# Kernel optimization log

Measured on AMD Instinct MI355X. Metric: run time of the kernel, lower is better.

The kernel has to match this reference:

```python
import jax, jax.numpy as jnp
import numpy as np

B, D, H, W = 16, 256, 32, 32
M = 2048


def setup_inputs() -> dict:
    key = jax.random.key(0)
    kz, ke = jax.random.split(key)
    z = jax.random.normal(kz, (B, D, H, W), dtype=jnp.float32)
    e = jax.random.normal(ke, (M, D), dtype=jnp.float32)
    return {"z": z, "e": e}


def reference(z, e):
    # flatten (B, D, H, W) -> (N, D), matching permute(0,2,3,1).reshape(-1, D)
    zf = jnp.transpose(z, (0, 2, 3, 1)).reshape(-1, z.shape[1])  # (N, D)
    # squared L2 distance via GEMM expansion: ||z||^2 + ||e||^2 - 2 z.e^T
    z_sq = jnp.sum(zf * zf, axis=1, keepdims=True)        # (N, 1)
    e_sq = jnp.sum(e * e, axis=1)                          # (M,)
    cross = jnp.einsum('nd,md->nm', zf, e)                 # (N, M)
    distance = jnp.maximum(z_sq + e_sq[None, :] - 2.0 * cross, 0.0)  # (N, M)
    # loss: mean over codes of min over flattened z vectors (min along dim 0)
    loss = jnp.mean(jnp.min(distance, axis=0))
    return distance, loss
```

## Files before the change

kernel.cpp:

```cpp
#include <hip/hip_runtime.h>

typedef __attribute__((ext_vector_type(8))) short bf16x8;
typedef __attribute__((ext_vector_type(4))) float f32x4;

#define NTOT 16384
#define MCODES 2048
#define DDIM 256

__device__ __forceinline__ unsigned short f2bf(float f) {
  union { float f; unsigned u; } v; v.f = f;
  unsigned r = v.u + 0x7FFFu + ((v.u >> 16) & 1u);
  return (unsigned short)(r >> 16);
}

#define GLOAD16(gptr, lptr) \
  __builtin_amdgcn_global_load_lds((const __attribute__((address_space(1))) void*)(gptr), \
                                   (__attribute__((address_space(3))) void*)(lptr), 16, 0, 0)

__global__ void prep_e_k(const float* __restrict__ e, unsigned short* __restrict__ ebf,
                         float* __restrict__ esq, unsigned* __restrict__ colmin,
                         float* __restrict__ zsq) {
  if (blockIdx.x < 64) zsq[blockIdx.x * 256 + threadIdx.x] = 0.0f;
  int row = blockIdx.x * 4 + (threadIdx.x >> 6);
  int lane = threadIdx.x & 63;
  const float4 v = *(const float4*)(e + (size_t)row * DDIM + lane * 4);
  ushort4 o;
  o.x = f2bf(v.x); o.y = f2bf(v.y); o.z = f2bf(v.z); o.w = f2bf(v.w);
  *(ushort4*)(ebf + (size_t)row * DDIM + lane * 4) = o;
  float s = v.x * v.x + v.y * v.y + v.z * v.z + v.w * v.w;
  #pragma unroll
  for (int off = 32; off; off >>= 1) s += __shfl_xor(s, off, 64);
  if (lane == 0) {
    esq[row] = s;
    colmin[row] = 0x7F800000u;
  }
}

__global__ void trans_zsq_k(const float* __restrict__ z, unsigned short* __restrict__ zf,
                            float* __restrict__ zsq) {
  __shared__ float t[64][65];
  const int b = blockIdx.z, d0 = blockIdx.x * 64, hw0 = blockIdx.y * 64;
  const int tid = threadIdx.x;
  {
    const int dl = tid >> 4, hwl = (tid & 15) * 4;
    const float* src = z + (size_t)b * 262144 + (size_t)(d0 + dl) * 1024 + hw0 + hwl;
    #pragma unroll
    for (int it = 0; it < 4; ++it) {
      float4 v = *(const float4*)(src + (size_t)it * 16 * 1024);
      *(float4*)&t[it * 16 + dl][hwl] = v;
    }
  }
  __syncthreads();
  const int hwl = tid >> 3;
  const int dl = (tid & 7) * 8;
  #pragma unroll
  for (int p = 0; p < 2; ++p) {
    const int hw = p * 32 + hwl;
    float vv[8];
    float s = 0.0f;
    #pragma unroll
    for (int u = 0; u < 8; ++u) { vv[u] = t[dl + u][hw]; s += vv[u] * vv[u]; }
    bf16x8 pk;
    #pragma unroll
    for (int u = 0; u < 8; ++u) pk[u] = (short)f2bf(vv[u]);
    const size_t n = (size_t)b * 1024 + hw0 + hw;
    *(bf16x8*)(zf + n * DDIM + d0 + dl) = pk;
    s += __shfl_xor(s, 1, 64);
    s += __shfl_xor(s, 2, 64);
    s += __shfl_xor(s, 4, 64);
    if ((tid & 7) == 0) atomicAdd(zsq + n, s);
  }
}

__global__ __launch_bounds__(256, 2) void gemm_k(
    const unsigned short* __restrict__ A,
    const unsigned short* __restrict__ B,
    const float* __restrict__ zsq, const float* __restrict__ esq,
    unsigned* __restrict__ colmin, float* __restrict__ out) {
  __shared__ unsigned short lds[2][2 * 128 * 64];
  const int tid = threadIdx.x;
  const int wave = tid >> 6, lane = tid & 63;
  const int wm = wave >> 1, wn = wave & 1;
  const int row0 = blockIdx.y * 128, col0 = blockIdx.x * 128;

  const int sr = tid >> 3;
  const int scs = ((tid & 7) * 8) ^ ((sr & 7) * 8);
  size_t aOff[4], bOff[4];
  #pragma unroll
  for (int c = 0; c < 4; ++c) {
    aOff[c] = (size_t)(row0 + c * 32 + sr) * DDIM + scs;
    bOff[c] = (size_t)(col0 + c * 32 + sr) * DDIM + scs;
  }

  const int rA = wm * 64 + (lane & 15);
  const int rB = wn * 64 + (lane & 15);
  const int slot = (lane >> 4) * 16;
  const int swz = (lane & 7) << 4;

  f32x4 acc[4][4] = {};

  #define STAGE(buf, k0)                                                    \
    {                                                                       \
      unsigned short* la = &lds[buf][0];                                    \
      unsigned short* lb = &lds[buf][8192];                                 \
      _Pragma("unroll")                                                     \
      for (int c = 0; c < 4; ++c) {                                         \
        GLOAD16(A + aOff[c] + (k0), la + c * 2048 + wave * 512);            \
        GLOAD16(B + bOff[c] + (k0), lb + c * 2048 + wave * 512);            \
      }                                                                     \
    }

  STAGE(0, 0);
  __syncthreads();
  #pragma unroll
  for (int t = 0; t < 4; ++t) {
    const int cur = t & 1;
    if (t < 3) STAGE(cur ^ 1, (t + 1) * 64);
    const char* pA = (const char*)&lds[cur][0];
    const char* pB = (const char*)&lds[cur][8192];
    bf16x8 av[2][4], bv[2][4];
    #pragma unroll
    for (int kk = 0; kk < 2; ++kk) {
      #pragma unroll
      for (int i = 0; i < 4; ++i)
        av[kk][i] = *(const bf16x8*)(pA + (rA + i * 16) * 128 + ((kk * 64 + slot) ^ swz));
      #pragma unroll
      for (int j = 0; j < 4; ++j)
        bv[kk][j] = *(const bf16x8*)(pB + (rB + j * 16) * 128 + ((kk * 64 + slot) ^ swz));
    }
    #pragma unroll
    for (int kk = 0; kk < 2; ++kk)
      #pragma unroll
      for (int i = 0; i < 4; ++i)
        #pragma unroll
        for (int j = 0; j < 4; ++j)
          acc[i][j] = __builtin_amdgcn_mfma_f32_16x16x32_bf16(av[kk][i], bv[kk][j], acc[i][j], 0, 0, 0);
    if (t < 3) __syncthreads();
  }
  #undef STAGE

  const int r0 = lane >> 4, c = lane & 15;
  float cmin[4] = {3.4e38f, 3.4e38f, 3.4e38f, 3.4e38f};
  #pragma unroll
  for (int j = 0; j < 4; ++j) {
    const int col = col0 + wn * 64 + j * 16 + c;
    const float es = esq[col];
    #pragma unroll
    for (int i = 0; i < 4; ++i) {
      const int row = row0 + wm * 64 + i * 16 + r0 * 4;
      const float4 zs = *(const float4*)(zsq + row);
      const float d0 = fmaxf(zs.x + es - 2.0f * acc[i][j][0], 0.0f);
      const float d1 = fmaxf(zs.y + es - 2.0f * acc[i][j][1], 0.0f);
      const float d2 = fmaxf(zs.z + es - 2.0f * acc[i][j][2], 0.0f);
      const float d3 = fmaxf(zs.w + es - 2.0f * acc[i][j][3], 0.0f);
      __builtin_nontemporal_store(d0, &out[(size_t)(row + 0) * MCODES + col]);
      __builtin_nontemporal_store(d1, &out[(size_t)(row + 1) * MCODES + col]);
      __builtin_nontemporal_store(d2, &out[(size_t)(row + 2) * MCODES + col]);
      __builtin_nontemporal_store(d3, &out[(size_t)(row + 3) * MCODES + col]);
      cmin[j] = fminf(cmin[j], fminf(fminf(d0, d1), fminf(d2, d3)));
    }
  }
  #pragma unroll
  for (int j = 0; j < 4; ++j) {
    float m = cmin[j];
    m = fminf(m, __shfl_xor(m, 16, 64));
    m = fminf(m, __shfl_xor(m, 32, 64));
    if (lane < 16) {
      const int col = col0 + wn * 64 + j * 16 + lane;
      atomicMin(colmin + col, __float_as_uint(m));
    }
  }
}

__global__ void loss_k(const unsigned* __restrict__ colmin, float* __restrict__ loss) {
  __shared__ float sdata[4];
  int t = threadIdx.x;
  float s = 0.0f;
  for (int i = t; i < MCODES; i += 256) s += __uint_as_float(colmin[i]);
  #pragma unroll
  for (int off = 32; off; off >>= 1) s += __shfl_down(s, off, 64);
  if ((t & 63) == 0) sdata[t >> 6] = s;
  __syncthreads();
  if (t == 0) loss[0] = (sdata[0] + sdata[1] + sdata[2] + sdata[3]) * (1.0f / (float)MCODES);
}

extern "C" void kernel_launch(void* const* d_in, const int* in_sizes, int n_in,
                              void* d_out, int out_size, void* d_ws, size_t ws_size,
                              hipStream_t stream) {
  const float* z = (const float*)d_in[0];
  const float* e = (const float*)d_in[1];
  float* out = (float*)d_out;

  float* ws = (float*)d_ws;
  float* zsq = ws;
  float* esq = ws + NTOT;
  unsigned* colmin = (unsigned*)(ws + NTOT + MCODES);
  unsigned short* ebf = (unsigned short*)(ws + NTOT + 2 * MCODES);
  unsigned short* zf = ebf + (size_t)MCODES * DDIM;

  prep_e_k<<<MCODES / 4, 256, 0, stream>>>(e, ebf, esq, colmin, zsq);
  trans_zsq_k<<<dim3(4, 16, 16), 256, 0, stream>>>(z, zf, zsq);
  gemm_k<<<dim3(MCODES / 128, NTOT / 128), 256, 0, stream>>>(zf, ebf, zsq, esq, colmin, out);
  loss_k<<<1, 256, 0, stream>>>(colmin, out + (size_t)NTOT * MCODES);
}
```

Measured before the change: 184.6 us.

## Fuse z transpose, bf16 cast and norm into GEMM A-tile loading

Removes the separate transpose/zsq kernel. The GEMM now reads fp32 z directly in NCHW layout, converts it to bf16 in registers, writes it into swizzled LDS and accumulates the row norms on the fly. The B operand (codebook) is read straight from global/L2 into registers instead of being staged through LDS. A block-index swizzle is added for L2 locality. This saves a kernel launch and the zf round trip. In exchange, each of the 16 column tiles re-reads and re-converts the fp32 z tile, and the B operand loses LDS reuse.

```diff
diff --git a/kernel.cpp b/kernel.cpp
--- a/kernel.cpp
+++ b/kernel.cpp
@@ -13,14 +13,8 @@
   return (unsigned short)(r >> 16);
 }
 
-#define GLOAD16(gptr, lptr) \
-  __builtin_amdgcn_global_load_lds((const __attribute__((address_space(1))) void*)(gptr), \
-                                   (__attribute__((address_space(3))) void*)(lptr), 16, 0, 0)
-
 __global__ void prep_e_k(const float* __restrict__ e, unsigned short* __restrict__ ebf,
-                         float* __restrict__ esq, unsigned* __restrict__ colmin,
-                         float* __restrict__ zsq) {
-  if (blockIdx.x < 64) zsq[blockIdx.x * 256 + threadIdx.x] = 0.0f;
+                         float* __restrict__ esq, unsigned* __restrict__ colmin) {
   int row = blockIdx.x * 4 + (threadIdx.x >> 6);
   int lane = threadIdx.x & 63;
   const float4 v = *(const float4*)(e + (size_t)row * DDIM + lane * 4);
@@ -36,97 +30,84 @@
   }
 }
 
-__global__ void trans_zsq_k(const float* __restrict__ z, unsigned short* __restrict__ zf,
-                            float* __restrict__ zsq) {
-  __shared__ float t[64][65];
-  const int b = blockIdx.z, d0 = blockIdx.x * 64, hw0 = blockIdx.y * 64;
-  const int tid = threadIdx.x;
-  {
-    const int dl = tid >> 4, hwl = (tid & 15) * 4;
-    const float* src = z + (size_t)b * 262144 + (size_t)(d0 + dl) * 1024 + hw0 + hwl;
-    #pragma unroll
-    for (int it = 0; it < 4; ++it) {
-      float4 v = *(const float4*)(src + (size_t)it * 16 * 1024);
-      *(float4*)&t[it * 16 + dl][hwl] = v;
-    }
-  }
-  __syncthreads();
-  const int hwl = tid >> 3;
-  const int dl = (tid & 7) * 8;
-  #pragma unroll
-  for (int p = 0; p < 2; ++p) {
-    const int hw = p * 32 + hwl;
-    float vv[8];
-    float s = 0.0f;
-    #pragma unroll
-    for (int u = 0; u < 8; ++u) { vv[u] = t[dl + u][hw]; s += vv[u] * vv[u]; }
-    bf16x8 pk;
-    #pragma unroll
-    for (int u = 0; u < 8; ++u) pk[u] = (short)f2bf(vv[u]);
-    const size_t n = (size_t)b * 1024 + hw0 + hw;
-    *(bf16x8*)(zf + n * DDIM + d0 + dl) = pk;
-    s += __shfl_xor(s, 1, 64);
-    s += __shfl_xor(s, 2, 64);
-    s += __shfl_xor(s, 4, 64);
-    if ((tid & 7) == 0) atomicAdd(zsq + n, s);
-  }
-}
+__global__ __launch_bounds__(256) void gemm_k(
+    const float* __restrict__ z,
+    const unsigned short* __restrict__ ebf,
+    const float* __restrict__ esq,
+    unsigned* __restrict__ colmin, float* __restrict__ out) {
+  __shared__ __align__(16) unsigned short As[2][128 * 64];
+  __shared__ __align__(16) float zsqt[2][128];
 
-__global__ __launch_bounds__(256, 2) void gemm_k(
-    const unsigned short* __restrict__ A,
-    const unsigned short* __restrict__ B,
-    const float* __restrict__ zsq, const float* __restrict__ esq,
-    unsigned* __restrict__ colmin, float* __restrict__ out) {
-  __shared__ unsigned short lds[2][2 * 128 * 64];
   const int tid = threadIdx.x;
   const int wave = tid >> 6, lane = tid & 63;
   const int wm = wave >> 1, wn = wave & 1;
-  const int row0 = blockIdx.y * 128, col0 = blockIdx.x * 128;
 
-  const int sr = tid >> 3;
-  const int scs = ((tid & 7) * 8) ^ ((sr & 7) * 8);
-  size_t aOff[4], bOff[4];
+  const int bid = blockIdx.x;
+  const int swz = (bid & 7) * 256 + (bid >> 3);
+  const int col0 = (swz & 15) * 128;
+  const int row0 = (swz >> 4) * 128;
+  const int bb = row0 >> 10, hw0 = row0 & 1023;
+
+  const int hw = tid & 127;
+  const int kdb = (tid >> 7) * 32;
+  const float* zsrc = z + (size_t)bb * 262144 + (size_t)kdb * 1024 + hw0 + hw;
+  unsigned wb[4];
   #pragma unroll
-  for (int c = 0; c < 4; ++c) {
-    aOff[c] = (size_t)(row0 + c * 32 + sr) * DDIM + scs;
-    bOff[c] = (size_t)(col0 + c * 32 + sr) * DDIM + scs;
-  }
+  for (int g = 0; g < 4; ++g)
+    wb[g] = hw * 128 + ((((kdb + 8 * g) * 2) ^ ((hw & 7) << 4)));
 
   const int rA = wm * 64 + (lane & 15);
-  const int rB = wn * 64 + (lane & 15);
   const int slot = (lane >> 4) * 16;
-  const int swz = (lane & 7) << 4;
+  const int aswz = (lane & 7) << 4;
 
+  const unsigned short* bp0 = ebf + (size_t)(col0 + wn * 64 + (lane & 15)) * DDIM + (lane >> 4) * 8;
+
+  float regA[32];
+  float zacc = 0.0f;
   f32x4 acc[4][4] = {};
 
-  #define STAGE(buf, k0)                                                    \
+  #define ALOAD(t)                                                          \
     {                                                                       \
-      unsigned short* la = &lds[buf][0];                                    \
-      unsigned short* lb = &lds[buf][8192];                                 \
+      const float* p_ = zsrc + (size_t)(t) * 64 * 1024;                     \
       _Pragma("unroll")                                                     \
-      for (int c = 0; c < 4; ++c) {                                         \
-        GLOAD16(A + aOff[c] + (k0), la + c * 2048 + wave * 512);            \
-        GLOAD16(B + bOff[c] + (k0), lb + c * 2048 + wave * 512);            \
+      for (int u = 0; u < 32; ++u) regA[u] = p_[(size_t)u * 1024];          \
+    }
+
+  #define AWRITE(buf)                                                       \
+    {                                                                       \
+      char* la_ = (char*)&As[buf][0];                                       \
+      _Pragma("unroll")                                                     \
+      for (int g = 0; g < 4; ++g) {                                         \
+        bf16x8 pk_;                                                         \
+        _Pragma("unroll")                                                   \
+        for (int u = 0; u < 8; ++u) {                                       \
+          float v_ = regA[g * 8 + u];                                       \
+          zacc += v_ * v_;                                                  \
+          pk_[u] = (short)f2bf(v_);                                         \
+        }                                                                   \
+        *(bf16x8*)(la_ + wb[g]) = pk_;                                      \
       }                                                                     \
     }
 
-  STAGE(0, 0);
+  ALOAD(0);
+  AWRITE(0);
   __syncthreads();
+
   #pragma unroll
   for (int t = 0; t < 4; ++t) {
     const int cur = t & 1;
-    if (t < 3) STAGE(cur ^ 1, (t + 1) * 64);
-    const char* pA = (const char*)&lds[cur][0];
-    const char* pB = (const char*)&lds[cur][8192];
+    if (t < 3) ALOAD(t + 1);
+
     bf16x8 av[2][4], bv[2][4];
+    const char* pA = (const char*)&As[cur][0];
     #pragma unroll
     for (int kk = 0; kk < 2; ++kk) {
       #pragma unroll
       for (int i = 0; i < 4; ++i)
-        av[kk][i] = *(const bf16x8*)(pA + (rA + i * 16) * 128 + ((kk * 64 + slot) ^ swz));
+        av[kk][i] = *(const bf16x8*)(pA + (rA + i * 16) * 128 + ((kk * 64 + slot) ^ aswz));
       #pragma unroll
       for (int j = 0; j < 4; ++j)
-        bv[kk][j] = *(const bf16x8*)(pB + (rB + j * 16) * 128 + ((kk * 64 + slot) ^ swz));
+        bv[kk][j] = *(const bf16x8*)(bp0 + (size_t)t * 64 + kk * 32 + (size_t)j * 16 * DDIM);
     }
     #pragma unroll
     for (int kk = 0; kk < 2; ++kk)
@@ -135,9 +116,17 @@
         #pragma unroll
         for (int j = 0; j < 4; ++j)
           acc[i][j] = __builtin_amdgcn_mfma_f32_16x16x32_bf16(av[kk][i], bv[kk][j], acc[i][j], 0, 0, 0);
-    if (t < 3) __syncthreads();
+
+    if (t < 3) {
+      AWRITE(cur ^ 1);
+      __syncthreads();
+    }
   }
-  #undef STAGE
+  #undef ALOAD
+  #undef AWRITE
+
+  zsqt[tid >> 7][hw] = zacc;
+  __syncthreads();
 
   const int r0 = lane >> 4, c = lane & 15;
   float cmin[4] = {3.4e38f, 3.4e38f, 3.4e38f, 3.4e38f};
@@ -147,12 +136,14 @@
     const float es = esq[col];
     #pragma unroll
     for (int i = 0; i < 4; ++i) {
-      const int row = row0 + wm * 64 + i * 16 + r0 * 4;
-      const float4 zs = *(const float4*)(zsq + row);
-      const float d0 = fmaxf(zs.x + es - 2.0f * acc[i][j][0], 0.0f);
-      const float d1 = fmaxf(zs.y + es - 2.0f * acc[i][j][1], 0.0f);
-      const float d2 = fmaxf(zs.z + es - 2.0f * acc[i][j][2], 0.0f);
-      const float d3 = fmaxf(zs.w + es - 2.0f * acc[i][j][3], 0.0f);
+      const int lr = wm * 64 + i * 16 + r0 * 4;
+      const int row = row0 + lr;
+      const float4 za = *(const float4*)&zsqt[0][lr];
+      const float4 zb = *(const float4*)&zsqt[1][lr];
+      const float d0 = fmaxf(za.x + zb.x + es - 2.0f * acc[i][j][0], 0.0f);
+      const float d1 = fmaxf(za.y + zb.y + es - 2.0f * acc[i][j][1], 0.0f);
+      const float d2 = fmaxf(za.z + zb.z + es - 2.0f * acc[i][j][2], 0.0f);
+      const float d3 = fmaxf(za.w + zb.w + es - 2.0f * acc[i][j][3], 0.0f);
       __builtin_nontemporal_store(d0, &out[(size_t)(row + 0) * MCODES + col]);
       __builtin_nontemporal_store(d1, &out[(size_t)(row + 1) * MCODES + col]);
       __builtin_nontemporal_store(d2, &out[(size_t)(row + 2) * MCODES + col]);
@@ -192,14 +183,11 @@
   float* out = (float*)d_out;
 
   float* ws = (float*)d_ws;
-  float* zsq = ws;
-  float* esq = ws + NTOT;
-  unsigned* colmin = (unsigned*)(ws + NTOT + MCODES);
-  unsigned short* ebf = (unsigned short*)(ws + NTOT + 2 * MCODES);
-  unsigned short* zf = ebf + (size_t)MCODES * DDIM;
+  float* esq = ws;
+  unsigned* colmin = (unsigned*)(ws + MCODES);
+  unsigned short* ebf = (unsigned short*)(ws + 2 * MCODES);
 
-  prep_e_k<<<MCODES / 4, 256, 0, stream>>>(e, ebf, esq, colmin, zsq);
-  trans_zsq_k<<<dim3(4, 16, 16), 256, 0, stream>>>(z, zf, zsq);
-  gemm_k<<<dim3(MCODES / 128, NTOT / 128), 256, 0, stream>>>(zf, ebf, zsq, esq, colmin, out);
+  prep_e_k<<<MCODES / 4, 256, 0, stream>>>(e, ebf, esq, colmin);
+  gemm_k<<<2048, 256, 0, stream>>>(z, ebf, esq, colmin, out);
   loss_k<<<1, 256, 0, stream>>>(colmin, out + (size_t)NTOT * MCODES);
 }
```

After: 243.8 us. 1.32x slower.

## Shrink GEMM K-tile to 32, raise occupancy, remap blocks per XCD

Applied to the files above, without the earlier changes.

The GEMM K-step drops from 64 to 32, which halves LDS per stage (16 KB double-buffered instead of 32 KB) so launch bounds can ask for 3 blocks per CU. A new swizzle matches the narrower 64-byte rows. The 2D grid becomes a 1D grid of 2048 blocks. Each XCD (selected by blockIdx & 7) gets a contiguous band of output rows, so A tiles are shared in that XCD's L2. In exchange there are twice as many barriers and stages, and the 3-block bound may constrain registers.

```diff
diff --git a/kernel.cpp b/kernel.cpp
--- a/kernel.cpp
+++ b/kernel.cpp
@@ -72,70 +72,64 @@
   }
 }
 
-__global__ __launch_bounds__(256, 2) void gemm_k(
+__global__ __launch_bounds__(256, 3) void gemm_k(
     const unsigned short* __restrict__ A,
     const unsigned short* __restrict__ B,
     const float* __restrict__ zsq, const float* __restrict__ esq,
     unsigned* __restrict__ colmin, float* __restrict__ out) {
-  __shared__ unsigned short lds[2][2 * 128 * 64];
+  __shared__ __align__(16) unsigned short As[2][128 * 32];
+  __shared__ __align__(16) unsigned short Bs[2][128 * 32];
+
   const int tid = threadIdx.x;
   const int wave = tid >> 6, lane = tid & 63;
   const int wm = wave >> 1, wn = wave & 1;
-  const int row0 = blockIdx.y * 128, col0 = blockIdx.x * 128;
 
-  const int sr = tid >> 3;
-  const int scs = ((tid & 7) * 8) ^ ((sr & 7) * 8);
-  size_t aOff[4], bOff[4];
-  #pragma unroll
-  for (int c = 0; c < 4; ++c) {
-    aOff[c] = (size_t)(row0 + c * 32 + sr) * DDIM + scs;
-    bOff[c] = (size_t)(col0 + c * 32 + sr) * DDIM + scs;
-  }
+  const int s_ = blockIdx.x >> 3, xcd = blockIdx.x & 7;
+  const int col0 = (s_ & 15) * 128;
+  const int row0 = ((s_ >> 4) + xcd * 16) * 128;
 
-  const int rA = wm * 64 + (lane & 15);
-  const int rB = wn * 64 + (lane & 15);
-  const int slot = (lane >> 4) * 16;
-  const int swz = (lane & 7) << 4;
+  const int sr_ = wave * 32 + (lane >> 2);
+  const int csw = ((lane & 3) ^ (sr_ & 3)) * 8;
+  const size_t aOff0 = (size_t)(row0 + sr_) * DDIM + csw;
+  const size_t aOff1 = (size_t)(row0 + sr_ + 16) * DDIM + csw;
+  const size_t bOff0 = (size_t)(col0 + sr_) * DDIM + csw;
+  const size_t bOff1 = (size_t)(col0 + sr_ + 16) * DDIM + csw;
+
+  const int fr = lane & 15;
+  const int axor = ((lane >> 4) << 4) ^ ((fr & 3) << 4);
 
   f32x4 acc[4][4] = {};
 
-  #define STAGE(buf, k0)                                                    \
-    {                                                                       \
-      unsigned short* la = &lds[buf][0];                                    \
-      unsigned short* lb = &lds[buf][8192];                                 \
-      _Pragma("unroll")                                                     \
-      for (int c = 0; c < 4; ++c) {                                         \
-        GLOAD16(A + aOff[c] + (k0), la + c * 2048 + wave * 512);            \
-        GLOAD16(B + bOff[c] + (k0), lb + c * 2048 + wave * 512);            \
-      }                                                                     \
+  #define STAGE(buf, k0)                                                        \
+    {                                                                           \
+      GLOAD16(A + aOff0 + (k0), (unsigned short*)As[buf] + wave * 1024);        \
+      GLOAD16(A + aOff1 + (k0), (unsigned short*)As[buf] + wave * 1024 + 512);  \
+      GLOAD16(B + bOff0 + (k0), (unsigned short*)Bs[buf] + wave * 1024);        \
+      GLOAD16(B + bOff1 + (k0), (unsigned short*)Bs[buf] + wave * 1024 + 512);  \
     }
 
   STAGE(0, 0);
   __syncthreads();
+
   #pragma unroll
-  for (int t = 0; t < 4; ++t) {
+  for (int t = 0; t < 8; ++t) {
     const int cur = t & 1;
-    if (t < 3) STAGE(cur ^ 1, (t + 1) * 64);
-    const char* pA = (const char*)&lds[cur][0];
-    const char* pB = (const char*)&lds[cur][8192];
-    bf16x8 av[2][4], bv[2][4];
+    if (t < 7) STAGE(cur ^ 1, (t + 1) * 32);
+    const char* pA = (const char*)As[cur];
+    const char* pB = (const char*)Bs[cur];
+    bf16x8 av[4], bv[4];
     #pragma unroll
-    for (int kk = 0; kk < 2; ++kk) {
-      #pragma unroll
-      for (int i = 0; i < 4; ++i)
-        av[kk][i] = *(const bf16x8*)(pA + (rA + i * 16) * 128 + ((kk * 64 + slot) ^ swz));
+    for (int i = 0; i < 4; ++i)
+      av[i] = *(const bf16x8*)(pA + (wm * 64 + i * 16 + fr) * 64 + axor);
+    #pragma unroll
+    for (int j = 0; j < 4; ++j)
+      bv[j] = *(const bf16x8*)(pB + (wn * 64 + j * 16 + fr) * 64 + axor);
+    #pragma unroll
+    for (int i = 0; i < 4; ++i)
       #pragma unroll
       for (int j = 0; j < 4; ++j)
-        bv[kk][j] = *(const bf16x8*)(pB + (rB + j * 16) * 128 + ((kk * 64 + slot) ^ swz));
-    }
-    #pragma unroll
-    for (int kk = 0; kk < 2; ++kk)
-      #pragma unroll
-      for (int i = 0; i < 4; ++i)
-        #pragma unroll
-        for (int j = 0; j < 4; ++j)
-          acc[i][j] = __builtin_amdgcn_mfma_f32_16x16x32_bf16(av[kk][i], bv[kk][j], acc[i][j], 0, 0, 0);
-    if (t < 3) __syncthreads();
+        acc[i][j] = __builtin_amdgcn_mfma_f32_16x16x32_bf16(av[i], bv[j], acc[i][j], 0, 0, 0);
+    if (t < 7) __syncthreads();
   }
   #undef STAGE
 
@@ -200,6 +194,6 @@
 
   prep_e_k<<<MCODES / 4, 256, 0, stream>>>(e, ebf, esq, colmin, zsq);
   trans_zsq_k<<<dim3(4, 16, 16), 256, 0, stream>>>(z, zf, zsq);
-  gemm_k<<<dim3(MCODES / 128, NTOT / 128), 256, 0, stream>>>(zf, ebf, zsq, esq, colmin, out);
+  gemm_k<<<2048, 256, 0, stream>>>(zf, ebf, zsq, esq, colmin, out);
   loss_k<<<1, 256, 0, stream>>>(colmin, out + (size_t)NTOT * MCODES);
 }
```

New measurement: 185.2 us. No clear change (+0.3%).
